# Kernel optimization log

Measured on AMD Instinct MI355X. Metric: run time of the kernel, lower is better.

## Reference

```python
import jax, jax.numpy as jnp
import numpy as np

SPATIAL = ((100, 134), (50, 67), (25, 34), (13, 17))
LEN = sum(h * w for h, w in SPATIAL)   # 17821
D, H, L, P = 384, 8, 4, 4
DH = D // H                            # 48
U = D // 3                             # unit_dim = 128
EPS = 1e-5


def _ln(x, g, b):
    m = jnp.mean(x, -1, keepdims=True)
    v = jnp.mean((x - m) ** 2, -1, keepdims=True)
    return (x - m) * jax.lax.rsqrt(v + EPS) * g + b


def _ffn(t, w1, b1, w2, b2, g, b):
    t2 = jax.nn.relu(t @ w1.T + b1) @ w2.T + b2
    return _ln(t + t2, g, b)


def _msda_core(value, loc, attn):
    # value [B,Lv,H,DH]; loc [B,Lq,H,L,P,2] normalized to [0,1]; attn [B,Lq,H,L,P]
    B = value.shape[0]
    Lq = loc.shape[1]
    out = jnp.zeros((B, H, Lq, DH), value.dtype)
    start = 0
    for lvl, (Hl, Wl) in enumerate(SPATIAL):
        n = Hl * Wl
        v = value[:, start:start + n].transpose(0, 2, 1, 3)        # [B,H,n,DH]
        # grid_sample(align_corners=False) semantics: pixel coord = loc*W - 0.5
        x = loc[:, :, :, lvl, :, 0] * Wl - 0.5                      # [B,Lq,H,P]
        y = loc[:, :, :, lvl, :, 1] * Hl - 0.5
        x0 = jnp.floor(x); y0 = jnp.floor(y)
        dx = x - x0; dy = y - y0
        x0i = x0.astype(jnp.int32); y0i = y0.astype(jnp.int32)
        acc = jnp.zeros((B, H, Lq, P, DH), value.dtype)
        corners = ((0, 0, (1 - dx) * (1 - dy)), (1, 0, dx * (1 - dy)),
                   (0, 1, (1 - dx) * dy), (1, 1, dx * dy))
        for ox, oy, w in corners:
            xi = x0i + ox; yi = y0i + oy
            valid = ((xi >= 0) & (xi < Wl) & (yi >= 0) & (yi < Hl)).astype(value.dtype)
            idx = jnp.clip(yi, 0, Hl - 1) * Wl + jnp.clip(xi, 0, Wl - 1)
            idx_t = idx.transpose(0, 2, 1, 3).reshape(B, H, Lq * P)
            g = jnp.take_along_axis(v, idx_t[..., None], axis=2).reshape(B, H, Lq, P, DH)
            acc = acc + g * (w * valid).transpose(0, 2, 1, 3)[..., None]
        out = out + (acc * attn[:, :, :, lvl].transpose(0, 2, 1, 3)[..., None]).sum(axis=3)
        start += n
    return out.transpose(0, 2, 1, 3).reshape(B, Lq, D)


def setup_inputs() -> dict:
    key = jax.random.key(0)
    ks = jax.random.split(key, 16)
    rn = lambda k, s, sc=1.0: jax.random.normal(k, s, jnp.float32) * sc
    inp = {}
    inp['src'] = rn(ks[0], (1, LEN, D))
    inp['space_query'] = rn(ks[1], (1, 1, 2 * U))
    inp['chann_query'] = rn(ks[2], (1, 1, 2 * U))
    inp['pos'] = rn(ks[3], (1, LEN, D))
    inp['reference_points'] = jax.random.uniform(ks[4], (1, LEN, L, 2), jnp.float32)
    inp['spatial_shapes'] = jnp.array(SPATIAL, jnp.int32)
    starts = np.cumsum([0] + [h * w for h, w in SPATIAL[:-1]])
    inp['level_start_index'] = jnp.array(starts, jnp.int32)
    inp['padding_mask'] = jnp.zeros((1, LEN), bool)
    # MSDeformAttn params (torch Linear convention: W is [out_features, in_features])
    inp['W_off'] = rn(ks[5], (H * L * P * 2, D), 0.01)
    inp['b_off'] = rn(ks[6], (H * L * P * 2,), 0.1)
    inp['W_attn'] = rn(ks[7], (H * L * P, D), D ** -0.5)
    inp['b_attn'] = jnp.zeros((H * L * P,), jnp.float32)
    inp['W_val'] = rn(ks[8], (D, D), D ** -0.5)
    inp['b_val'] = jnp.zeros((D,), jnp.float32)
    inp['W_out'] = rn(ks[9], (D, D), D ** -0.5)
    inp['b_out'] = jnp.zeros((D,), jnp.float32)
    # norm1_xy / norm1_zd
    inp['g1xy'] = jnp.ones((2 * U,), jnp.float32); inp['b1xy'] = jnp.zeros((2 * U,), jnp.float32)
    inp['g1zd'] = jnp.ones((U,), jnp.float32); inp['b1zd'] = jnp.zeros((U,), jnp.float32)
    # ffn_xy: Linear(2U,2U) -> relu -> Linear(2U,2U), residual + LN
    inp['fxy_w1'] = rn(ks[10], (2 * U, 2 * U), (2 * U) ** -0.5); inp['fxy_b1'] = jnp.zeros((2 * U,), jnp.float32)
    inp['fxy_w2'] = rn(ks[11], (2 * U, 2 * U), (2 * U) ** -0.5); inp['fxy_b2'] = jnp.zeros((2 * U,), jnp.float32)
    inp['fxy_g'] = jnp.ones((2 * U,), jnp.float32); inp['fxy_b'] = jnp.zeros((2 * U,), jnp.float32)
    # ffn_zd: Linear(U,U) -> relu -> Linear(U,U), residual + LN
    inp['fzd_w1'] = rn(ks[12], (U, U), U ** -0.5); inp['fzd_b1'] = jnp.zeros((U,), jnp.float32)
    inp['fzd_w2'] = rn(ks[13], (U, U), U ** -0.5); inp['fzd_b2'] = jnp.zeros((U,), jnp.float32)
    inp['fzd_g'] = jnp.ones((U,), jnp.float32); inp['fzd_b'] = jnp.zeros((U,), jnp.float32)
    return inp


def reference(src, space_query, chann_query, pos, reference_points, spatial_shapes,
              level_start_index, padding_mask,
              W_off, b_off, W_attn, b_attn, W_val, b_val, W_out, b_out,
              g1xy, b1xy, g1zd, b1zd,
              fxy_w1, fxy_b1, fxy_w2, fxy_b2, fxy_g, fxy_b,
              fzd_w1, fzd_b1, fzd_w2, fzd_b2, fzd_g, fzd_b):
    B, Lq, _ = src.shape
    q = src + pos                                        # with_pos_embed
    value = src @ W_val.T + b_val
    value = jnp.where(padding_mask[..., None], 0.0, value).reshape(B, Lq, H, DH)
    off = (q @ W_off.T + b_off).reshape(B, Lq, H, L, P, 2)
    attn = jax.nn.softmax((q @ W_attn.T + b_attn).reshape(B, Lq, H, L * P), -1)
    attn = attn.reshape(B, Lq, H, L, P)
    wh = jnp.array([[w, h] for h, w in SPATIAL], src.dtype)         # [L,2] as (W,H)
    loc = reference_points[:, :, None, :, None, :] + off / wh[None, None, None, :, None, :]
    src2 = _msda_core(value, loc, attn) @ W_out.T + b_out
    src_xy = _ln(src[..., :2 * U] + src2[..., :2 * U], g1xy, b1xy)
    src_zd = _ln(src[..., 2 * U:] + src2[..., 2 * U:], g1zd, b1zd)
    src_xy = _ffn(src_xy, fxy_w1, fxy_b1, fxy_w2, fxy_b2, fxy_g, fxy_b)
    src_zd = _ffn(src_zd, fzd_w1, fzd_b1, fzd_w2, fzd_b2, fzd_g, fzd_b)
    return jnp.concatenate([src_xy, src_zd], axis=-1)
```

## Files before the change

### kernel.cpp

```cpp
#include <hip/hip_runtime.h>
#include <math.h>

#define LEN 17821
#define DMODEL 384
#define NHEAD 8
#define DHEAD 48
#define WSZ (384 * 384)

typedef float floatx4 __attribute__((ext_vector_type(4)));
typedef short shortx8 __attribute__((ext_vector_type(8)));
typedef unsigned short ushort;

__device__ inline ushort f2bf(float f) {
    unsigned int u = __float_as_uint(f);
    u += 0x7FFFu + ((u >> 16) & 1u);
    return (ushort)(u >> 16);
}
__device__ inline float bf2f(ushort s) {
    return __uint_as_float(((unsigned int)s) << 16);
}

__device__ inline floatx4 mfma_bf16(shortx8 a, shortx8 b, floatx4 c) {
    return __builtin_amdgcn_mfma_f32_16x16x32_bf16(a, b, c, 0, 0, 0);
}

__global__ __launch_bounds__(256)
void prep_w(const float* __restrict__ Wval, const float* __restrict__ Woff,
            const float* __restrict__ Wattn, const float* __restrict__ Wout,
            const float* __restrict__ w1xy, const float* __restrict__ w1zd,
            const float* __restrict__ w2xy, const float* __restrict__ w2zd,
            ushort* __restrict__ wv, ushort* __restrict__ woa,
            ushort* __restrict__ wo, ushort* __restrict__ w1b,
            ushort* __restrict__ w2b) {
    int idx = blockIdx.x * 256 + threadIdx.x;
    if (idx >= WSZ) return;
    int job = blockIdx.y;
    float v; ushort* dst;
    if (job <= 1) {
        int n = idx / 384, k = idx - n * 384;
        if (job == 0) { v = Wval[idx]; dst = wv; }
        else {
            v = n < 256 ? Woff[n * 384 + k] : Wattn[(n - 256) * 384 + k];
            dst = woa;
        }
    } else {
        int e = idx & 7;
        int lane = (idx >> 3) & 63;
        int t = idx >> 9;
        int j = t % 3;
        int t2 = t / 3;
        int wv8 = t2 & 7;
        int hs = t2 >> 3;
        int l15 = lane & 15, quad = lane >> 4;
        int row = wv8 * 48 + j * 16 + l15;
        int k = hs * 32 + quad * 8 + e;
        if (job == 2) { v = Wout[row * 384 + k]; dst = wo; }
        else if (job == 3) {
            v = row < 256 ? (k < 256 ? w1xy[row * 256 + k] : 0.f)
                          : (k >= 256 ? w1zd[(row - 256) * 128 + (k - 256)] : 0.f);
            dst = w1b;
        } else {
            v = row < 256 ? (k < 256 ? w2xy[row * 256 + k] : 0.f)
                          : (k >= 256 ? w2zd[(row - 256) * 128 + (k - 256)] : 0.f);
            dst = w2b;
        }
    }
    dst[idx] = f2bf(v);
}

__global__ __launch_bounds__(384)
void prep_b(const float* __restrict__ boff, const float* __restrict__ battn,
            const float* __restrict__ b1xy, const float* __restrict__ b1zd,
            const float* __restrict__ b2xy, const float* __restrict__ b2zd,
            const float* __restrict__ g1xy, const float* __restrict__ be1xy,
            const float* __restrict__ g1zd, const float* __restrict__ be1zd,
            const float* __restrict__ g2xy, const float* __restrict__ be2xy,
            const float* __restrict__ g2zd, const float* __restrict__ be2zd,
            float* __restrict__ boa, float* __restrict__ b1c,
            float* __restrict__ b2c, float* __restrict__ l1g,
            float* __restrict__ l1b, float* __restrict__ l2g,
            float* __restrict__ l2b) {
    int i = threadIdx.x;
    bool lo = i < 256; int j = lo ? i : i - 256;
    boa[i] = lo ? boff[i] : battn[j];
    b1c[i] = lo ? b1xy[i] : b1zd[j];
    b2c[i] = lo ? b2xy[i] : b2zd[j];
    l1g[i] = lo ? g1xy[i] : g1zd[j];
    l1b[i] = lo ? be1xy[i] : be1zd[j];
    l2g[i] = lo ? g2xy[i] : g2zd[j];
    l2b[i] = lo ? be2xy[i] : be2zd[j];
}

__global__ __launch_bounds__(256)
void cvt_add(const float* __restrict__ src, const float* __restrict__ pos,
             ushort* __restrict__ src_bf, ushort* __restrict__ q_bf, int n8) {
    int i = blockIdx.x * 256 + threadIdx.x;
    if (i >= n8) return;
    float4 s0 = ((const float4*)src)[i * 2], s1 = ((const float4*)src)[i * 2 + 1];
    float4 p0 = ((const float4*)pos)[i * 2], p1 = ((const float4*)pos)[i * 2 + 1];
    shortx8 sb, qb;
    sb[0] = f2bf(s0.x); sb[1] = f2bf(s0.y); sb[2] = f2bf(s0.z); sb[3] = f2bf(s0.w);
    sb[4] = f2bf(s1.x); sb[5] = f2bf(s1.y); sb[6] = f2bf(s1.z); sb[7] = f2bf(s1.w);
    qb[0] = f2bf(s0.x + p0.x); qb[1] = f2bf(s0.y + p0.y);
    qb[2] = f2bf(s0.z + p0.z); qb[3] = f2bf(s0.w + p0.w);
    qb[4] = f2bf(s1.x + p1.x); qb[5] = f2bf(s1.y + p1.y);
    qb[6] = f2bf(s1.z + p1.z); qb[7] = f2bf(s1.w + p1.w);
    ((shortx8*)src_bf)[i] = sb;
    ((shortx8*)q_bf)[i] = qb;
}

#define TSV 128
#define LSTRIDE 40

__global__ __launch_bounds__(256)
void vq_gemm(const ushort* __restrict__ sbq, const ushort* __restrict__ qbq,
             const ushort* __restrict__ wv, const ushort* __restrict__ woa,
             const float* __restrict__ bval, const float* __restrict__ boa,
             ushort* __restrict__ vout, float* __restrict__ oaout) {
    __shared__ ushort As[TSV * LSTRIDE];
    __shared__ ushort Ws[TSV * LSTRIDE];
    bool job = blockIdx.x >= 3;
    int bx = job ? blockIdx.x - 3 : blockIdx.x;
    const ushort* A = job ? qbq : sbq;
    const ushort* W = job ? woa : wv;
    const float* bias = job ? boa : bval;
    int tid = threadIdx.x;
    int lane = tid & 63, wave = tid >> 6;
    int wr = (wave >> 1) * 64, wc = (wave & 1) * 64;
    int l15 = lane & 15, quad = lane >> 4;
    int srow = tid >> 1, shalf = tid & 1;
    int by = blockIdx.y;
    int garow = by * TSV + srow;
    bool avalid = garow < LEN;
    const ushort* ap = A + (size_t)(avalid ? garow : 0) * 384 + shalf * 16;
    const ushort* wp = W + (size_t)(bx * TSV + srow) * 384 + shalf * 16;
    ushort* as_dst = &As[srow * LSTRIDE + shalf * 16];
    ushort* ws_dst = &Ws[srow * LSTRIDE + shalf * 16];

    floatx4 acc[4][4];
    #pragma unroll
    for (int i = 0; i < 4; ++i)
        #pragma unroll
        for (int j = 0; j < 4; ++j)
            acc[i][j] = (floatx4){0.f, 0.f, 0.f, 0.f};

    shortx8 a0 = *(const shortx8*)(ap);
    shortx8 a1 = *(const shortx8*)(ap + 8);
    shortx8 w0 = *(const shortx8*)(wp);
    shortx8 w1 = *(const shortx8*)(wp + 8);

    for (int k0 = 0; k0 < 384; k0 += 32) {
        __syncthreads();
        *(shortx8*)(as_dst + 0) = a0;
        *(shortx8*)(as_dst + 8) = a1;
        *(shortx8*)(ws_dst + 0) = w0;
        *(shortx8*)(ws_dst + 8) = w1;
        __syncthreads();
        if (k0 + 32 < 384) {
            a0 = *(const shortx8*)(ap + k0 + 32);
            a1 = *(const shortx8*)(ap + k0 + 40);
            w0 = *(const shortx8*)(wp + k0 + 32);
            w1 = *(const shortx8*)(wp + k0 + 40);
        }
        shortx8 af[4], bfr[4];
        #pragma unroll
        for (int i = 0; i < 4; ++i)
            af[i] = *(shortx8*)&As[(wr + i * 16 + l15) * LSTRIDE + quad * 8];
        #pragma unroll
        for (int j = 0; j < 4; ++j)
            bfr[j] = *(shortx8*)&Ws[(wc + j * 16 + l15) * LSTRIDE + quad * 8];
        #pragma unroll
        for (int i = 0; i < 4; ++i)
            #pragma unroll
            for (int j = 0; j < 4; ++j)
                acc[i][j] = __builtin_amdgcn_mfma_f32_16x16x32_bf16(
                    af[i], bfr[j], acc[i][j], 0, 0, 0);
    }

    #pragma unroll
    for (int j = 0; j < 4; ++j) {
        int col = bx * TSV + wc + j * 16 + l15;
        float bv = bias[col];
        #pragma unroll
        for (int i = 0; i < 4; ++i) {
            #pragma unroll
            for (int r = 0; r < 4; ++r) {
                int row = by * TSV + wr + i * 16 + quad * 4 + r;
                if (row < LEN) {
                    float v = acc[i][j][r] + bv;
                    if (job) oaout[(size_t)row * 384 + col] = v;
                    else     vout[(size_t)row * 384 + col] = f2bf(v);
                }
            }
        }
    }
}

#define MTOK 8
__global__ __launch_bounds__(384)
void msda_v3(const ushort* __restrict__ value,
             const float* __restrict__ offattn,
             const float* __restrict__ refpts,
             ushort* __restrict__ out) {
    __shared__ int   sx0[MTOK * 128], sy0[MTOK * 128];
    __shared__ float sdx[MTOK * 128], sdy[MTOK * 128], saw[MTOK * 128];
    constexpr int Wi[4]  = {134, 67, 34, 17};
    constexpr int Hi[4]  = {100, 50, 25, 13};
    constexpr int STi[4] = {0, 13400, 16750, 17600};
    int t0 = blockIdx.x * MTOK;
    int tid = threadIdx.x;

    if (tid < MTOK * 8) {
        int ti = tid >> 3, h = tid & 7, t = t0 + ti;
        if (t < LEN) {
            const float* lg = offattn + (size_t)t * 384 + 256 + h * 16;
            float w[16], mx = -3.4e38f;
            #pragma unroll
            for (int s = 0; s < 16; ++s) { w[s] = lg[s]; mx = fmaxf(mx, w[s]); }
            float sum = 0.f;
            #pragma unroll
            for (int s = 0; s < 16; ++s) { w[s] = __expf(w[s] - mx); sum += w[s]; }
            float inv = 1.0f / sum;
            #pragma unroll
            for (int s = 0; s < 16; ++s) saw[ti * 128 + h * 16 + s] = w[s] * inv;
        }
    }
    for (int idx = tid; idx < MTOK * 128; idx += 384) {
        int ti = idx >> 7, rem = idx & 127, h = rem >> 4, p = rem & 15;
        int lvl = p >> 2, pp = p & 3;
        int t = t0 + ti;
        if (t < LEN) {
            float Wl = (float)Wi[lvl], Hl = (float)Hi[lvl];
            const float* op = offattn + (size_t)t * 384 + h * 32 + lvl * 8 + pp * 2;
            float ox = op[0], oy = op[1];
            float rx = refpts[(size_t)t * 8 + lvl * 2];
            float ry = refpts[(size_t)t * 8 + lvl * 2 + 1];
            float x = rx * Wl + ox - 0.5f;
            float y = ry * Hl + oy - 0.5f;
            float x0 = floorf(x), y0 = floorf(y);
            sx0[idx] = (int)x0; sy0[idx] = (int)y0;
            sdx[idx] = x - x0;  sdy[idx] = y - y0;
        }
    }
    __syncthreads();

    int ti = tid / 48;
    int r = tid - ti * 48;
    int h = r / 6;
    int c = r - h * 6;
    int t = t0 + ti;
    if (t >= LEN) return;
    const ushort* vb = value + h * DHEAD + c * 8;
    float a[8] = {};
    #pragma unroll
    for (int p = 0; p < 16; ++p) {
        const int lvl = p >> 2;
        const int Wl = Wi[lvl], Hl = Hi[lvl], st = STi[lvl];
        int base = ti * 128 + h * 16 + p;
        int x0 = sx0[base], y0 = sy0[base];
        float dx = sdx[base], dy = sdy[base], aw = saw[base];
        float cwv[4] = {(1.f - dx) * (1.f - dy), dx * (1.f - dy),
                        (1.f - dx) * dy, dx * dy};
        #pragma unroll
        for (int c2 = 0; c2 < 4; ++c2) {
            int xi = x0 + (c2 & 1), yi = y0 + (c2 >> 1);
            bool valid = (xi >= 0) & (xi < Wl) & (yi >= 0) & (yi < Hl);
            int xc = min(max(xi, 0), Wl - 1);
            int yc = min(max(yi, 0), Hl - 1);
            float s = valid ? aw * cwv[c2] : 0.f;
            shortx8 g = *(const shortx8*)(vb + (size_t)(st + yc * Wl + xc) * 384);
            #pragma unroll
            for (int k = 0; k < 8; ++k) a[k] += s * bf2f(g[k]);
        }
    }
    shortx8 o;
    #pragma unroll
    for (int k = 0; k < 8; ++k) o[k] = f2bf(a[k]);
    *(shortx8*)(out + (size_t)t * 384 + h * DHEAD + c * 8) = o;
}

#define MT 32
#define CST 392

#define GEMM384(WPTR)                                                         \
  {                                                                           \
    const ushort* wp_ = (WPTR) + wave * 1536 + lane * 8;                      \
    _Pragma("unroll")                                                         \
    for (int i_ = 0; i_ < 2; ++i_)                                            \
      _Pragma("unroll")                                                       \
      for (int j_ = 0; j_ < 3; ++j_) acc[i_][j_] = (floatx4){0.f,0.f,0.f,0.f};\
    shortx8 wcr[3], wnr[3];                                                   \
    _Pragma("unroll")                                                         \
    for (int j_ = 0; j_ < 3; ++j_)                                            \
      wcr[j_] = *(const shortx8*)(wp_ + j_ * 512);                            \
    _Pragma("unroll")                                                         \
    for (int hs = 0; hs < 12; ++hs) {                                         \
      if (hs < 11) {                                                          \
        _Pragma("unroll")                                                     \
        for (int j_ = 0; j_ < 3; ++j_)                                        \
          wnr[j_] = *(const shortx8*)(wp_ + (hs + 1) * 12288 + j_ * 512);     \
      }                                                                       \
      shortx8 a0 = *(shortx8*)&Cbuf[l15 * CST + hs * 32 + quad * 8];          \
      shortx8 a1 = *(shortx8*)&Cbuf[(16 + l15) * CST + hs * 32 + quad * 8];   \
      _Pragma("unroll")                                                       \
      for (int j_ = 0; j_ < 3; ++j_) {                                        \
        acc[0][j_] = mfma_bf16(a0, wcr[j_], acc[0][j_]);                      \
        acc[1][j_] = mfma_bf16(a1, wcr[j_], acc[1][j_]);                      \
      }                                                                       \
      if (hs < 11) {                                                          \
        _Pragma("unroll")                                                     \
        for (int j_ = 0; j_ < 3; ++j_) wcr[j_] = wnr[j_];                     \
      }                                                                       \
    }                                                                         \
  }

__global__ __launch_bounds__(512, 2)
void mega_kernel(const ushort* __restrict__ Amsda, const float* __restrict__ src,
                 const ushort* __restrict__ Wo, const ushort* __restrict__ W1,
                 const ushort* __restrict__ W2,
                 const float* __restrict__ bo, const float* __restrict__ b1c,
                 const float* __restrict__ b2c,
                 const float* __restrict__ l1g, const float* __restrict__ l1b,
                 const float* __restrict__ l2g, const float* __restrict__ l2b,
                 float* __restrict__ h1f, float* __restrict__ outp) {
    __shared__ __align__(16) ushort Cbuf[MT * CST];
    __shared__ __align__(16) floatx4 pst4[MT * 16];
    __shared__ __align__(16) floatx4 lnf[MT];

    int tid = threadIdx.x;
    int lane = tid & 63, wave = tid >> 6;
    int l15 = lane & 15, quad = lane >> 4;
    int wcol = wave * 48;
    int by0 = blockIdx.x * MT;

    floatx4 acc[2][3];

    #pragma unroll
    for (int cix = 0; cix < 3; ++cix) {
        int idx = cix * 512 + tid;
        int row = idx / 48, c = idx - row * 48;
        int gr = min(by0 + row, LEN - 1);
        *(shortx8*)(Cbuf + row * CST + c * 8) =
            *(const shortx8*)(Amsda + (size_t)gr * 384 + c * 8);
    }
    __syncthreads();

    GEMM384(Wo);
    __syncthreads();

    #pragma unroll
    for (int j = 0; j < 3; ++j) {
        int col = wcol + j * 16 + l15;
        float bv = bo[col];
        #pragma unroll
        for (int i = 0; i < 2; ++i)
            #pragma unroll
            for (int rr = 0; rr < 4; ++rr) {
                int row = i * 16 + quad * 4 + rr;
                int gr = min(by0 + row, LEN - 1);
                float x = acc[i][j][rr] + bv + src[(size_t)gr * 384 + col];
                Cbuf[row * CST + col] = f2bf(x);
            }
    }
    __syncthreads();

    {
        int row = tid >> 4, part = tid & 15;
        float sx = 0.f, qx = 0.f, sz = 0.f, qz = 0.f;
        #pragma unroll
        for (int m = 0; m < 3; ++m) {
            int c0 = part * 24 + m * 8;
            shortx8 v = *(shortx8*)(Cbuf + row * CST + c0);
            float cs = 0.f, cq = 0.f;
            #pragma unroll
            for (int e = 0; e < 8; ++e) { float x = bf2f(v[e]); cs += x; cq += x * x; }
            if (c0 < 256) { sx += cs; qx += cq; } else { sz += cs; qz += cq; }
        }
        pst4[row * 16 + part] = (floatx4){sx, qx, sz, qz};
    }
    __syncthreads();
    if (tid < MT) {
        floatx4 s = (floatx4){0.f, 0.f, 0.f, 0.f};
        #pragma unroll
        for (int p = 0; p < 16; ++p) s += pst4[tid * 16 + p];
        float mx = s[0] / 256.f, vx = s[1] / 256.f - mx * mx;
        float mz = s[2] / 128.f, vz = s[3] / 128.f - mz * mz;
        lnf[tid] = (floatx4){mx, rsqrtf(vx + 1e-5f), mz, rsqrtf(vz + 1e-5f)};
    }
    __syncthreads();
    {
        int row = tid >> 4, part = tid & 15;
        int gr = by0 + row;
        floatx4 L = lnf[row];
        #pragma unroll
        for (int m = 0; m < 3; ++m) {
            int c0 = part * 24 + m * 8;
            bool isxy = c0 < 256;
            float mean = isxy ? L[0] : L[2];
            float inv  = isxy ? L[1] : L[3];
            shortx8 v = *(shortx8*)(Cbuf + row * CST + c0);
            float4 g0 = *(const float4*)(l1g + c0), g1 = *(const float4*)(l1g + c0 + 4);
            float4 e0 = *(const float4*)(l1b + c0), e1 = *(const float4*)(l1b + c0 + 4);
            float gg[8] = {g0.x, g0.y, g0.z, g0.w, g1.x, g1.y, g1.z, g1.w};
            float ee[8] = {e0.x, e0.y, e0.z, e0.w, e1.x, e1.y, e1.z, e1.w};
            float h[8];
            shortx8 hb;
            #pragma unroll
            for (int e = 0; e < 8; ++e) {
                h[e] = (bf2f(v[e]) - mean) * inv * gg[e] + ee[e];
                hb[e] = f2bf(h[e]);
            }
            *(shortx8*)(Cbuf + row * CST + c0) = hb;
            if (gr < LEN) {
                *(float4*)(h1f + (size_t)gr * 384 + c0)     = make_float4(h[0], h[1], h[2], h[3]);
                *(float4*)(h1f + (size_t)gr * 384 + c0 + 4) = make_float4(h[4], h[5], h[6], h[7]);
            }
        }
    }
    __syncthreads();

    GEMM384(W1);
    __syncthreads();
    #pragma unroll
    for (int j = 0; j < 3; ++j) {
        int col = wcol + j * 16 + l15;
        float bv = b1c[col];
        #pragma unroll
        for (int i = 0; i < 2; ++i)
            #pragma unroll
            for (int rr = 0; rr < 4; ++rr) {
                int row = i * 16 + quad * 4 + rr;
                Cbuf[row * CST + col] = f2bf(fmaxf(acc[i][j][rr] + bv, 0.f));
            }
    }
    __syncthreads();

    GEMM384(W2);
    __syncthreads();
    #pragma unroll
    for (int j = 0; j < 3; ++j) {
        int col = wcol + j * 16 + l15;
        float bv = b2c[col];
        #pragma unroll
        for (int i = 0; i < 2; ++i)
            #pragma unroll
            for (int rr = 0; rr < 4; ++rr) {
                int row = i * 16 + quad * 4 + rr;
                int gr = min(by0 + row, LEN - 1);
                float x = acc[i][j][rr] + bv + h1f[(size_t)gr * 384 + col];
                Cbuf[row * CST + col] = f2bf(x);
            }
    }
    __syncthreads();

    {
        int row = tid >> 4, part = tid & 15;
        float sx = 0.f, qx = 0.f, sz = 0.f, qz = 0.f;
        #pragma unroll
        for (int m = 0; m < 3; ++m) {
            int c0 = part * 24 + m * 8;
            shortx8 v = *(shortx8*)(Cbuf + row * CST + c0);
            float cs = 0.f, cq = 0.f;
            #pragma unroll
            for (int e = 0; e < 8; ++e) { float x = bf2f(v[e]); cs += x; cq += x * x; }
            if (c0 < 256) { sx += cs; qx += cq; } else { sz += cs; qz += cq; }
        }
        pst4[row * 16 + part] = (floatx4){sx, qx, sz, qz};
    }
    __syncthreads();
    if (tid < MT) {
        floatx4 s = (floatx4){0.f, 0.f, 0.f, 0.f};
        #pragma unroll
        for (int p = 0; p < 16; ++p) s += pst4[tid * 16 + p];
        float mx = s[0] / 256.f, vx = s[1] / 256.f - mx * mx;
        float mz = s[2] / 128.f, vz = s[3] / 128.f - mz * mz;
        lnf[tid] = (floatx4){mx, rsqrtf(vx + 1e-5f), mz, rsqrtf(vz + 1e-5f)};
    }
    __syncthreads();
    {
        int row = tid >> 4, part = tid & 15;
        int gr = by0 + row;
        if (gr < LEN) {
            floatx4 L = lnf[row];
            #pragma unroll
            for (int m = 0; m < 3; ++m) {
                int c0 = part * 24 + m * 8;
                bool isxy = c0 < 256;
                float mean = isxy ? L[0] : L[2];
                float inv  = isxy ? L[1] : L[3];
                shortx8 v = *(shortx8*)(Cbuf + row * CST + c0);
                float4 g0 = *(const float4*)(l2g + c0), g1 = *(const float4*)(l2g + c0 + 4);
                float4 e0 = *(const float4*)(l2b + c0), e1 = *(const float4*)(l2b + c0 + 4);
                float gg[8] = {g0.x, g0.y, g0.z, g0.w, g1.x, g1.y, g1.z, g1.w};
                float ee[8] = {e0.x, e0.y, e0.z, e0.w, e1.x, e1.y, e1.z, e1.w};
                float h[8];
                #pragma unroll
                for (int e = 0; e < 8; ++e)
                    h[e] = (bf2f(v[e]) - mean) * inv * gg[e] + ee[e];
                *(float4*)(outp + (size_t)gr * 384 + c0)     = make_float4(h[0], h[1], h[2], h[3]);
                *(float4*)(outp + (size_t)gr * 384 + c0 + 4) = make_float4(h[4], h[5], h[6], h[7]);
            }
        }
    }
}

extern "C" void kernel_launch(void* const* d_in, const int* in_sizes, int n_in,
                              void* d_out, int out_size, void* d_ws, size_t ws_size,
                              hipStream_t stream) {
    const float* src    = (const float*)d_in[0];
    const float* pos    = (const float*)d_in[3];
    const float* refpts = (const float*)d_in[4];
    const float* W_off  = (const float*)d_in[8];
    const float* b_off  = (const float*)d_in[9];
    const float* W_attn = (const float*)d_in[10];
    const float* b_attn = (const float*)d_in[11];
    const float* W_val  = (const float*)d_in[12];
    const float* b_val  = (const float*)d_in[13];
    const float* W_out  = (const float*)d_in[14];
    const float* b_out  = (const float*)d_in[15];
    const float* g1xy = (const float*)d_in[16]; const float* b1xy = (const float*)d_in[17];
    const float* g1zd = (const float*)d_in[18]; const float* b1zd = (const float*)d_in[19];
    const float* fxy_w1 = (const float*)d_in[20]; const float* fxy_b1 = (const float*)d_in[21];
    const float* fxy_w2 = (const float*)d_in[22]; const float* fxy_b2 = (const float*)d_in[23];
    const float* fxy_g  = (const float*)d_in[24]; const float* fxy_b  = (const float*)d_in[25];
    const float* fzd_w1 = (const float*)d_in[26]; const float* fzd_b1 = (const float*)d_in[27];
    const float* fzd_w2 = (const float*)d_in[28]; const float* fzd_b2 = (const float*)d_in[29];
    const float* fzd_g  = (const float*)d_in[30]; const float* fzd_b  = (const float*)d_in[31];

    float* out = (float*)d_out;
    size_t Rn = (size_t)LEN * DMODEL;

    float* f0 = (float*)d_ws;
    ushort* sb = (ushort*)(f0 + Rn);
    ushort* s0 = sb;
    ushort* s1 = sb + Rn;
    ushort* s2 = sb + 2 * Rn;
    ushort* s3 = sb + 3 * Rn;
    ushort* wv  = sb + 4 * Rn;
    ushort* woa = wv + WSZ;
    ushort* wo  = woa + WSZ;
    ushort* w1b = wo + WSZ;
    ushort* w2b = w1b + WSZ;
    float* bp = (float*)(w2b + WSZ);
    float* boa = bp;        float* b1c = bp + 384;  float* b2c = bp + 768;
    float* l1g = bp + 1152; float* l1b = bp + 1536;
    float* l2g = bp + 1920; float* l2b = bp + 2304;

    prep_w<<<dim3((WSZ + 255) / 256, 5), 256, 0, stream>>>(
        W_val, W_off, W_attn, W_out, fxy_w1, fzd_w1, fxy_w2, fzd_w2,
        wv, woa, wo, w1b, w2b);
    prep_b<<<1, 384, 0, stream>>>(b_off, b_attn, fxy_b1, fzd_b1, fxy_b2, fzd_b2,
                                  g1xy, b1xy, g1zd, b1zd, fxy_g, fxy_b, fzd_g, fzd_b,
                                  boa, b1c, b2c, l1g, l1b, l2g, l2b);

    int n8 = (int)(Rn / 8);
    cvt_add<<<(n8 + 255) / 256, 256, 0, stream>>>(src, pos, s0, s1, n8);

    vq_gemm<<<dim3(6, (LEN + TSV - 1) / TSV), 256, 0, stream>>>(
        s0, s1, wv, woa, b_val, boa, s2, f0);

    msda_v3<<<(LEN + MTOK - 1) / MTOK, 384, 0, stream>>>(s2, f0, refpts, s3);

    mega_kernel<<<(LEN + MT - 1) / MT, 512, 0, stream>>>(
        s3, src, wo, w1b, w2b, b_out, b1c, b2c,
        l1g, l1b, l2g, l2b, f0, out);
}
```

Measured before the change: 309.5 us.

## Remap MSDA blocks per XCD and precompute corner indices and weights

```diff
diff --git a/kernel.cpp b/kernel.cpp
--- a/kernel.cpp
+++ b/kernel.cpp
@@ -8,6 +8,7 @@
 #define WSZ (384 * 384)
 
 typedef float floatx4 __attribute__((ext_vector_type(4)));
+typedef float floatx2 __attribute__((ext_vector_type(2)));
 typedef short shortx8 __attribute__((ext_vector_type(8)));
 typedef unsigned short ushort;
 
@@ -197,17 +198,24 @@
 }
 
 #define MTOK 8
+#define NXCD 8
 __global__ __launch_bounds__(384)
-void msda_v3(const ushort* __restrict__ value,
+void msda_v4(const ushort* __restrict__ value,
              const float* __restrict__ offattn,
              const float* __restrict__ refpts,
-             ushort* __restrict__ out) {
-    __shared__ int   sx0[MTOK * 128], sy0[MTOK * 128];
-    __shared__ float sdx[MTOK * 128], sdy[MTOK * 128], saw[MTOK * 128];
+             ushort* __restrict__ out, int nwg) {
+    __shared__ float saw[MTOK * 128];
+    __shared__ int   si4[MTOK * 128][4];
+    __shared__ float sw4[MTOK * 128][4];
     constexpr int Wi[4]  = {134, 67, 34, 17};
     constexpr int Hi[4]  = {100, 50, 25, 13};
     constexpr int STi[4] = {0, 13400, 16750, 17600};
-    int t0 = blockIdx.x * MTOK;
+
+    int orig = blockIdx.x;
+    int q = nwg / NXCD, r = nwg % NXCD;
+    int xcd = orig % NXCD, ci = orig / NXCD;
+    int bid = (xcd < r ? xcd * (q + 1) : r * (q + 1) + (xcd - r) * q) + ci;
+    int t0 = bid * MTOK;
     int tid = threadIdx.x;
 
     if (tid < MTOK * 8) {
@@ -225,57 +233,77 @@
             for (int s = 0; s < 16; ++s) saw[ti * 128 + h * 16 + s] = w[s] * inv;
         }
     }
+    __syncthreads();
+
     for (int idx = tid; idx < MTOK * 128; idx += 384) {
         int ti = idx >> 7, rem = idx & 127, h = rem >> 4, p = rem & 15;
         int lvl = p >> 2, pp = p & 3;
         int t = t0 + ti;
         if (t < LEN) {
             float Wl = (float)Wi[lvl], Hl = (float)Hi[lvl];
+            const int Wli = Wi[lvl], Hli = Hi[lvl], st = STi[lvl];
             const float* op = offattn + (size_t)t * 384 + h * 32 + lvl * 8 + pp * 2;
             float ox = op[0], oy = op[1];
             float rx = refpts[(size_t)t * 8 + lvl * 2];
             float ry = refpts[(size_t)t * 8 + lvl * 2 + 1];
             float x = rx * Wl + ox - 0.5f;
             float y = ry * Hl + oy - 0.5f;
-            float x0 = floorf(x), y0 = floorf(y);
-            sx0[idx] = (int)x0; sy0[idx] = (int)y0;
-            sdx[idx] = x - x0;  sdy[idx] = y - y0;
+            float x0f = floorf(x), y0f = floorf(y);
+            int x0 = (int)x0f, y0 = (int)y0f;
+            float dx = x - x0f, dy = y - y0f;
+            float aw = saw[idx];
+            float cwv[4] = {(1.f - dx) * (1.f - dy), dx * (1.f - dy),
+                            (1.f - dx) * dy, dx * dy};
+            #pragma unroll
+            for (int c2 = 0; c2 < 4; ++c2) {
+                int xi = x0 + (c2 & 1), yi = y0 + (c2 >> 1);
+                bool valid = (xi >= 0) & (xi < Wli) & (yi >= 0) & (yi < Hli);
+                int xc = min(max(xi, 0), Wli - 1);
+                int yc = min(max(yi, 0), Hli - 1);
+                si4[idx][c2] = st + yc * Wli + xc;
+                sw4[idx][c2] = valid ? aw * cwv[c2] : 0.f;
+            }
         }
     }
     __syncthreads();
 
     int ti = tid / 48;
-    int r = tid - ti * 48;
-    int h = r / 6;
-    int c = r - h * 6;
+    int rr = tid - ti * 48;
+    int h = rr / 6;
+    int c = rr - h * 6;
     int t = t0 + ti;
     if (t >= LEN) return;
     const ushort* vb = value + h * DHEAD + c * 8;
-    float a[8] = {};
+    floatx2 a2[4] = {};
     #pragma unroll
     for (int p = 0; p < 16; ++p) {
-        const int lvl = p >> 2;
-        const int Wl = Wi[lvl], Hl = Hi[lvl], st = STi[lvl];
         int base = ti * 128 + h * 16 + p;
-        int x0 = sx0[base], y0 = sy0[base];
-        float dx = sdx[base], dy = sdy[base], aw = saw[base];
-        float cwv[4] = {(1.f - dx) * (1.f - dy), dx * (1.f - dy),
-                        (1.f - dx) * dy, dx * dy};
+        int4  I = *(const int4*)&si4[base][0];
+        float4 W4 = *(const float4*)&sw4[base][0];
+        const int   Iv[4] = {I.x, I.y, I.z, I.w};
+        const float Wv[4] = {W4.x, W4.y, W4.z, W4.w};
         #pragma unroll
         for (int c2 = 0; c2 < 4; ++c2) {
-            int xi = x0 + (c2 & 1), yi = y0 + (c2 >> 1);
-            bool valid = (xi >= 0) & (xi < Wl) & (yi >= 0) & (yi < Hl);
-            int xc = min(max(xi, 0), Wl - 1);
-            int yc = min(max(yi, 0), Hl - 1);
-            float s = valid ? aw * cwv[c2] : 0.f;
-            shortx8 g = *(const shortx8*)(vb + (size_t)(st + yc * Wl + xc) * 384);
-            #pragma unroll
-            for (int k = 0; k < 8; ++k) a[k] += s * bf2f(g[k]);
+            shortx8 g = *(const shortx8*)(vb + (size_t)Iv[c2] * 384);
+            float s = Wv[c2];
+            floatx2 s2 = {s, s};
+            const unsigned int* gu = (const unsigned int*)&g;
+            #pragma unroll
+            for (int q2 = 0; q2 < 4; ++q2) {
+                unsigned int u = gu[q2];
+                floatx2 gf;
+                gf[0] = __uint_as_float(u << 16);
+                gf[1] = __uint_as_float(u & 0xFFFF0000u);
+                a2[q2] += s2 * gf;
+            }
         }
     }
     shortx8 o;
     #pragma unroll
-    for (int k = 0; k < 8; ++k) o[k] = f2bf(a[k]);
+    for (int q2 = 0; q2 < 4; ++q2) {
+        o[q2 * 2]     = f2bf(a2[q2][0]);
+        o[q2 * 2 + 1] = f2bf(a2[q2][1]);
+    }
     *(shortx8*)(out + (size_t)t * 384 + h * DHEAD + c * 8) = o;
 }
 
@@ -559,7 +587,8 @@
     vq_gemm<<<dim3(6, (LEN + TSV - 1) / TSV), 256, 0, stream>>>(
         s0, s1, wv, woa, b_val, boa, s2, f0);
 
-    msda_v3<<<(LEN + MTOK - 1) / MTOK, 384, 0, stream>>>(s2, f0, refpts, s3);
+    int nwg = (LEN + MTOK - 1) / MTOK;
+    msda_v4<<<nwg, 384, 0, stream>>>(s2, f0, refpts, s3, nwg);
 
     mega_kernel<<<(LEN + MT - 1) / MT, 512, 0, stream>>>(
         s3, src, wo, w1b, w2b, b_out, b1c, b2c,
```

New measurement: 305.2 us. About the same (-1.4%).
